# Kernel optimization log

Measured on AMD Instinct MI355X. Metric: run time of the kernel, lower is better.

Reference implementation:

```python
import jax, jax.numpy as jnp
import numpy as np

EPS = 1e-6

def _layernorm(x, g, b):
    mu = jnp.mean(x, axis=-1, keepdims=True)
    var = jnp.mean(jnp.square(x - mu), axis=-1, keepdims=True)
    return (x - mu) * jax.lax.rsqrt(var + EPS) * g + b


def setup_inputs() -> dict:
    key = jax.random.key(0)
    ks = jax.random.split(key, 8)
    B, T, C, H, D = 4096, 64, 256, 4, 64
    s = 0.02
    return {
        "x": jax.random.normal(ks[0], (B, T, C), jnp.float32),
        "ln1_g": jnp.ones((C,), jnp.float32),
        "ln1_b": jnp.zeros((C,), jnp.float32),
        "Wq": jax.random.normal(ks[1], (H, C, D), jnp.float32) * s,
        "Wk": jax.random.normal(ks[2], (H, C, D), jnp.float32) * s,
        "Wv": jax.random.normal(ks[3], (H, C, D), jnp.float32) * s,
        "Wproj": jax.random.normal(ks[4], (C, C), jnp.float32) * s,
        "bproj": jnp.zeros((C,), jnp.float32),
        "ln2_g": jnp.ones((C,), jnp.float32),
        "ln2_b": jnp.zeros((C,), jnp.float32),
        "W1": jax.random.normal(ks[5], (C, 4 * C), jnp.float32) * s,
        "b1": jnp.zeros((4 * C,), jnp.float32),
        "W2": jax.random.normal(ks[6], (4 * C, C), jnp.float32) * s,
        "b2": jnp.zeros((C,), jnp.float32),
    }


def reference(x, ln1_g, ln1_b, Wq, Wk, Wv, Wproj, bproj, ln2_g, ln2_b, W1, b1, W2, b2):
    B, T, C = x.shape
    H, _, D = Wq.shape
    # --- self-attention on pre-LN input (dropout = identity at inference) ---
    h = _layernorm(x, ln1_g, ln1_b)
    q = jnp.einsum('btc,hcd->bhtd', h, Wq)
    k = jnp.einsum('btc,hcd->bhtd', h, Wk)
    v = jnp.einsum('btc,hcd->bhtd', h, Wv)
    scale = jax.lax.rsqrt(jnp.asarray(D, x.dtype))
    wei = jnp.einsum('bhtd,bhsd->bhts', q, k) * scale
    causal = jnp.tril(jnp.ones((T, T), bool))  # matches tril[:T,:T]
    wei = jnp.where(causal, wei, -jnp.inf)
    wei = jax.nn.softmax(wei, axis=-1)
    att = jnp.einsum('bhts,bhsd->bhtd', wei, v)
    att = att.transpose(0, 2, 1, 3).reshape(B, T, H * D)  # concat heads
    sa = att @ Wproj + bproj
    x = x + sa
    # --- feed-forward ---
    h2 = _layernorm(x, ln2_g, ln2_b)
    ff = jax.nn.relu(h2 @ W1 + b1) @ W2 + b2
    return x + ff
```

## Files before the change

### kernel.cpp

```cpp
#include <hip/hip_runtime.h>
#include <hip/hip_bf16.h>


typedef float v4f __attribute__((ext_vector_type(4)));
typedef int   v4i __attribute__((ext_vector_type(4)));
typedef float f4v __attribute__((ext_vector_type(4)));
typedef unsigned long long u64;

#define DEV static __device__ __forceinline__

DEV unsigned short f2bf(float f){
  return __builtin_bit_cast(unsigned short, __float2bfloat16(f));
}

DEV v4f mfma16(v4i a, v4i b, v4f c){
  asm("v_mfma_f32_16x16x32_bf16 %0, %1, %2, %0" : "+v"(c) : "v"(a), "v"(b));
  return c;
}
DEV v4f accfence(v4f c){
  asm("s_nop 7\n\ts_nop 3" : "+v"(c));
  return c;
}

DEV int hoff(int r, int c){ return r*512 + ((c*2) ^ ((r & 7) << 4)); }
DEV int koff(int r, int c){ return r*128 + ((c*2) ^ ((r & 7) << 4)); }
DEV int aoff(int r, int c){ return r*256 + ((c*2) ^ ((r & 7) << 4)); }

DEV u64 pack4(v4f v){
  return (u64)f2bf(v[0]) | ((u64)f2bf(v[1]) << 16)
       | ((u64)f2bf(v[2]) << 32) | ((u64)f2bf(v[3]) << 48);
}

DEV float rsum64(float v){
  #pragma unroll
  for (int k = 1; k < 64; k <<= 1) v += __shfl_xor(v, k);
  return v;
}
DEV float rsum16(float v){
  #pragma unroll
  for (int k = 1; k < 16; k <<= 1) v += __shfl_xor(v, k);
  return v;
}
DEV float rmax16(float v){
  #pragma unroll
  for (int k = 1; k < 16; k <<= 1) v = fmaxf(v, __shfl_xor(v, k));
  return v;
}

__global__ void prep_w(const float* __restrict__ Wq, const float* __restrict__ Wk,
                       const float* __restrict__ Wv, const float* __restrict__ Wp,
                       const float* __restrict__ W1, const float* __restrict__ W2,
                       unsigned short* __restrict__ ws){
  int t = blockIdx.x * 256 + threadIdx.x;
  float v;
  if (t < 196608){
    int seg = t >> 16, r = t & 65535;
    int c = r & 255, d = (r >> 8) & 63, h = r >> 14;
    const float* W = (seg == 0) ? Wq : ((seg == 1) ? Wk : Wv);
    v = W[h*16384 + c*64 + d];
  } else if (t < 262144){
    int r = t - 196608; int n = r >> 8, c = r & 255;
    v = Wp[c*256 + n];
  } else if (t < 524288){
    int r = t - 262144; int n = r >> 8, c = r & 255;
    v = W1[c*1024 + n];
  } else {
    int r = t - 524288; int n = r >> 10, k = r & 1023;
    v = W2[k*256 + n];
  }
  ws[t] = f2bf(v);
}

__global__ __launch_bounds__(256, 2) void attnproj_k(
    const float* __restrict__ x,
    const float* __restrict__ ln1g, const float* __restrict__ ln1b,
    const unsigned short* __restrict__ wqT,
    const unsigned short* __restrict__ wkT,
    const unsigned short* __restrict__ wvT,
    const unsigned short* __restrict__ wpT,
    const float* __restrict__ bpj,
    float* __restrict__ outp)
{
  __shared__ char smb[65536] __attribute__((aligned(16)));
  char* sm = smb;
  const int HLS = 0, QLS = 32768, KLS = 40960, VTLS = 49152, PATLS = 57344;

  const int b = blockIdx.x;
  const float* __restrict__ xb = x + (size_t)b * 16384;
  float* __restrict__ ob = outp + (size_t)b * 16384;
  const int tid = threadIdx.x;
  const int w = tid >> 6, l = tid & 63, m = l & 15, g = l >> 4;
  const v4f zf = {0.f, 0.f, 0.f, 0.f};

  {
    f4v lg = *(const f4v*)(ln1g + 4*l);
    f4v lb = *(const f4v*)(ln1b + 4*l);
    #pragma unroll
    for (int rr = 0; rr < 16; ++rr){
      int r = w*16 + rr;
      f4v xv = *(const f4v*)(xb + r*256 + 4*l);
      float s = xv[0]+xv[1]+xv[2]+xv[3];
      float q = xv[0]*xv[0]+xv[1]*xv[1]+xv[2]*xv[2]+xv[3]*xv[3];
      s = rsum64(s); q = rsum64(q);
      float mu = s * (1.f/256.f);
      float rs = rsqrtf(q * (1.f/256.f) - mu*mu + 1e-6f);
      u64 pk = 0;
      #pragma unroll
      for (int j = 0; j < 4; ++j){
        float hv = (xv[j] - mu) * rs * lg[j] + lb[j];
        pk |= (u64)f2bf(hv) << (16*j);
      }
      *(u64*)(sm + HLS + hoff(r, 4*l)) = pk;
    }
  }
  __syncthreads();

  v4f sa[4][4];
  #pragma unroll
  for (int i = 0; i < 4; ++i){
    #pragma unroll
    for (int j = 0; j < 4; ++j) sa[i][j] = zf;
  }

  #pragma unroll 1
  for (int hh = 0; hh < 4; ++hh){
    {
      const unsigned short* bq = wqT + hh*16384 + (w*16 + m)*256;
      const unsigned short* bk = wkT + hh*16384 + (w*16 + m)*256;
      const unsigned short* bv = wvT + hh*16384 + (w*16 + m)*256;
      v4f qa[4] = {zf,zf,zf,zf}, ka[4] = {zf,zf,zf,zf}, va[4] = {zf,zf,zf,zf};
      #pragma unroll
      for (int ks = 0; ks < 8; ++ks){
        int k0 = ks*32 + 8*g;
        v4i bq4 = *(const v4i*)(bq + k0);
        v4i bk4 = *(const v4i*)(bk + k0);
        v4i bv4 = *(const v4i*)(bv + k0);
        #pragma unroll
        for (int rt = 0; rt < 4; ++rt){
          v4i af = *(const v4i*)(sm + HLS + hoff(rt*16 + m, k0));
          qa[rt] = mfma16(af, bq4, qa[rt]);
          ka[rt] = mfma16(af, bk4, ka[rt]);
          va[rt] = mfma16(af, bv4, va[rt]);
        }
      }
      #pragma unroll
      for (int rt = 0; rt < 4; ++rt){
        qa[rt] = accfence(qa[rt]); ka[rt] = accfence(ka[rt]); va[rt] = accfence(va[rt]);
        #pragma unroll
        for (int j = 0; j < 4; ++j){
          *(unsigned short*)(sm + QLS + koff(rt*16 + 4*g + j, w*16 + m)) = f2bf(qa[rt][j]);
          *(unsigned short*)(sm + KLS + koff(rt*16 + 4*g + j, w*16 + m)) = f2bf(ka[rt][j]);
        }
        *(u64*)(sm + VTLS + koff(w*16 + m, rt*16 + 4*g)) = pack4(va[rt]);
      }
    }
    __syncthreads();

    {
      v4f s4[4] = {zf,zf,zf,zf};
      #pragma unroll
      for (int ks = 0; ks < 2; ++ks){
        int k0 = ks*32 + 8*g;
        v4i qf = *(const v4i*)(sm + QLS + koff(w*16 + m, k0));
        #pragma unroll
        for (int nt = 0; nt < 4; ++nt){
          v4i kf = *(const v4i*)(sm + KLS + koff(nt*16 + m, k0));
          s4[nt] = mfma16(qf, kf, s4[nt]);
        }
      }
      #pragma unroll
      for (int nt = 0; nt < 4; ++nt) s4[nt] = accfence(s4[nt]);
      float mx[4] = {-3e38f, -3e38f, -3e38f, -3e38f};
      #pragma unroll
      for (int nt = 0; nt < 4; ++nt){
        #pragma unroll
        for (int j = 0; j < 4; ++j){
          int t = w*16 + 4*g + j, ss = nt*16 + m;
          float z = s4[nt][j] * 0.125f;
          z = (ss <= t) ? z : -1e30f;
          s4[nt][j] = z;
          mx[j] = fmaxf(mx[j], z);
        }
      }
      #pragma unroll
      for (int j = 0; j < 4; ++j) mx[j] = rmax16(mx[j]);
      float sum[4] = {0.f, 0.f, 0.f, 0.f};
      #pragma unroll
      for (int nt = 0; nt < 4; ++nt){
        #pragma unroll
        for (int j = 0; j < 4; ++j){
          float p = __expf(s4[nt][j] - mx[j]);
          s4[nt][j] = p;
          sum[j] += p;
        }
      }
      #pragma unroll
      for (int j = 0; j < 4; ++j) sum[j] = 1.f / rsum16(sum[j]);
      #pragma unroll
      for (int nt = 0; nt < 4; ++nt){
        #pragma unroll
        for (int j = 0; j < 4; ++j)
          *(unsigned short*)(sm + PATLS + w*2048 + koff(4*g + j, nt*16 + m)) =
              f2bf(s4[nt][j] * sum[j]);
      }
      v4f av[4] = {zf,zf,zf,zf};
      #pragma unroll
      for (int ks = 0; ks < 2; ++ks){
        int k0 = ks*32 + 8*g;
        v4i pf = *(const v4i*)(sm + PATLS + w*2048 + koff(m, k0));
        #pragma unroll
        for (int nt = 0; nt < 4; ++nt){
          v4i vf = *(const v4i*)(sm + VTLS + koff(nt*16 + m, k0));
          av[nt] = mfma16(pf, vf, av[nt]);
        }
      }
      #pragma unroll
      for (int nt = 0; nt < 4; ++nt) av[nt] = accfence(av[nt]);
      #pragma unroll
      for (int nt = 0; nt < 4; ++nt){
        #pragma unroll
        for (int j = 0; j < 4; ++j)
          *(unsigned short*)(sm + PATLS + w*2048 + koff(4*g + j, nt*16 + m)) =
              f2bf(av[nt][j]);
      }
    }
    __syncthreads();

    #pragma unroll
    for (int ks = 0; ks < 2; ++ks){
      int k0 = ks*32 + 8*g;
      v4i af2[4];
      #pragma unroll
      for (int rt = 0; rt < 4; ++rt)
        af2[rt] = *(const v4i*)(sm + PATLS + rt*2048 + koff(m, k0));
      #pragma unroll
      for (int nt = 0; nt < 4; ++nt){
        v4i bp = *(const v4i*)(wpT + (w*64 + nt*16 + m)*256 + hh*64 + k0);
        #pragma unroll
        for (int rt = 0; rt < 4; ++rt) sa[rt][nt] = mfma16(af2[rt], bp, sa[rt][nt]);
      }
    }
  }

  {
    #pragma unroll
    for (int i = 0; i < 4; ++i){
      #pragma unroll
      for (int j = 0; j < 4; ++j) sa[i][j] = accfence(sa[i][j]);
    }
    float bp4[4];
    #pragma unroll
    for (int nt = 0; nt < 4; ++nt) bp4[nt] = bpj[w*64 + nt*16 + m];
    #pragma unroll
    for (int rt = 0; rt < 4; ++rt){
      #pragma unroll
      for (int j = 0; j < 4; ++j){
        int row = rt*16 + 4*g + j;
        #pragma unroll
        for (int nt = 0; nt < 4; ++nt){
          int col = w*64 + nt*16 + m;
          ob[row*256 + col] = xb[row*256 + col] + sa[rt][nt][j] + bp4[nt];
        }
      }
    }
  }
}

__global__ __launch_bounds__(256, 2) void mlp_k(
    const float* __restrict__ ln2g, const float* __restrict__ ln2b,
    const unsigned short* __restrict__ w1T,
    const float* __restrict__ b1,
    const unsigned short* __restrict__ w2T,
    const float* __restrict__ b2,
    float* __restrict__ outp)
{
  __shared__ char smb[65536] __attribute__((aligned(16)));
  char* sm = smb;
  const int HLS = 0;
  const int ACT0 = 32768, ACT1 = 49152;
  const int b = blockIdx.x;
  float* __restrict__ ob = outp + (size_t)b * 16384;
  const int tid = threadIdx.x;
  const int w = tid >> 6, l = tid & 63, m = l & 15, g = l >> 4;
  const v4f zf = {0.f, 0.f, 0.f, 0.f};

  {
    f4v lg = *(const f4v*)(ln2g + 4*l);
    f4v lb = *(const f4v*)(ln2b + 4*l);
    #pragma unroll
    for (int rr = 0; rr < 16; ++rr){
      int r = w*16 + rr;
      f4v xv = *(const f4v*)(ob + r*256 + 4*l);
      float s = xv[0]+xv[1]+xv[2]+xv[3];
      float q = xv[0]*xv[0]+xv[1]*xv[1]+xv[2]*xv[2]+xv[3]*xv[3];
      s = rsum64(s); q = rsum64(q);
      float mu = s * (1.f/256.f);
      float rs = rsqrtf(q * (1.f/256.f) - mu*mu + 1e-6f);
      u64 pk = 0;
      #pragma unroll
      for (int j = 0; j < 4; ++j){
        float hv = (xv[j] - mu) * rs * lg[j] + lb[j];
        pk |= (u64)f2bf(hv) << (16*j);
      }
      *(u64*)(sm + HLS + hoff(r, 4*l)) = pk;
    }
  }
  __syncthreads();

  v4f ff[4][4];
  #pragma unroll
  for (int i = 0; i < 4; ++i){
    #pragma unroll
    for (int j = 0; j < 4; ++j) ff[i][j] = zf;
  }

  #pragma unroll 1
  for (int ch = 0; ch < 8; ++ch){
    const int ACT = (ch & 1) ? ACT1 : ACT0;
    v4f a1[4][2];
    #pragma unroll
    for (int i = 0; i < 4; ++i){ a1[i][0] = zf; a1[i][1] = zf; }
    const unsigned short* w1a = w1T + (ch*128 + w*32 +      m)*256;
    const unsigned short* w1b = w1T + (ch*128 + w*32 + 16 + m)*256;
    #pragma unroll
    for (int ks = 0; ks < 8; ++ks){
      int k0 = ks*32 + 8*g;
      v4i bw0 = *(const v4i*)(w1a + k0);
      v4i bw1 = *(const v4i*)(w1b + k0);
      #pragma unroll
      for (int rt = 0; rt < 4; ++rt){
        v4i af = *(const v4i*)(sm + HLS + hoff(rt*16 + m, k0));
        a1[rt][0] = mfma16(af, bw0, a1[rt][0]);
        a1[rt][1] = mfma16(af, bw1, a1[rt][1]);
      }
    }
    float b1v[2] = { b1[ch*128 + w*32 + m], b1[ch*128 + w*32 + 16 + m] };
    #pragma unroll
    for (int i = 0; i < 4; ++i){ a1[i][0] = accfence(a1[i][0]); a1[i][1] = accfence(a1[i][1]); }
    #pragma unroll
    for (int rt = 0; rt < 4; ++rt){
      #pragma unroll
      for (int j = 0; j < 4; ++j){
        int row = rt*16 + 4*g + j;
        #pragma unroll
        for (int nt = 0; nt < 2; ++nt){
          float v = fmaxf(a1[rt][nt][j] + b1v[nt], 0.f);
          *(unsigned short*)(sm + ACT + aoff(row, w*32 + nt*16 + m)) = f2bf(v);
        }
      }
    }
    __syncthreads();
    #pragma unroll
    for (int ks = 0; ks < 4; ++ks){
      int k0 = ks*32 + 8*g;
      v4i af[4];
      #pragma unroll
      for (int rt = 0; rt < 4; ++rt)
        af[rt] = *(const v4i*)(sm + ACT + aoff(rt*16 + m, k0));
      #pragma unroll
      for (int nt = 0; nt < 4; ++nt){
        v4i bw = *(const v4i*)(w2T + (w*64 + nt*16 + m)*1024 + ch*128 + k0);
        #pragma unroll
        for (int rt = 0; rt < 4; ++rt) ff[rt][nt] = mfma16(af[rt], bw, ff[rt][nt]);
      }
    }
  }

  {
    float b2v[4];
    #pragma unroll
    for (int nt = 0; nt < 4; ++nt) b2v[nt] = b2[w*64 + nt*16 + m];
    #pragma unroll
    for (int i = 0; i < 4; ++i){
      #pragma unroll
      for (int j = 0; j < 4; ++j) ff[i][j] = accfence(ff[i][j]);
    }
    #pragma unroll
    for (int rt = 0; rt < 4; ++rt){
      #pragma unroll
      for (int j = 0; j < 4; ++j){
        int row = rt*16 + 4*g + j;
        #pragma unroll
        for (int nt = 0; nt < 4; ++nt){
          int col = w*64 + nt*16 + m;
          ob[row*256 + col] += ff[rt][nt][j] + b2v[nt];
        }
      }
    }
  }
}

extern "C" void kernel_launch(void* const* d_in, const int* in_sizes, int n_in,
                              void* d_out, int out_size, void* d_ws, size_t ws_size,
                              hipStream_t stream) {
  const float* x    = (const float*)d_in[0];
  const float* ln1g = (const float*)d_in[1];
  const float* ln1b = (const float*)d_in[2];
  const float* Wq   = (const float*)d_in[3];
  const float* Wk   = (const float*)d_in[4];
  const float* Wv   = (const float*)d_in[5];
  const float* Wp   = (const float*)d_in[6];
  const float* bpj  = (const float*)d_in[7];
  const float* ln2g = (const float*)d_in[8];
  const float* ln2b = (const float*)d_in[9];
  const float* W1   = (const float*)d_in[10];
  const float* b1   = (const float*)d_in[11];
  const float* W2   = (const float*)d_in[12];
  const float* b2   = (const float*)d_in[13];
  unsigned short* ws = (unsigned short*)d_ws;
  float* outp = (float*)d_out;

  prep_w<<<3072, 256, 0, stream>>>(Wq, Wk, Wv, Wp, W1, W2, ws);
  attnproj_k<<<4096, 256, 0, stream>>>(x, ln1g, ln1b,
                                       ws, ws + 65536, ws + 131072, ws + 196608,
                                       bpj, outp);
  mlp_k<<<4096, 256, 0, stream>>>(ln2g, ln2b, ws + 262144, b1,
                                  ws + 524288, b2, outp);
}
```

Baseline: 965.8 us.

## Retile MLP kernel to 128 rows per 512-thread block, add lightweight barriers

Result: faster. 897.8 us (-7.0%).

```diff
diff --git a/kernel.cpp b/kernel.cpp
--- a/kernel.cpp
+++ b/kernel.cpp
@@ -13,6 +13,10 @@
   return __builtin_bit_cast(unsigned short, __float2bfloat16(f));
 }
 
+DEV void bar(){
+  asm volatile("s_waitcnt lgkmcnt(0)\n\ts_barrier" ::: "memory");
+}
+
 DEV v4f mfma16(v4i a, v4i b, v4f c){
   asm("v_mfma_f32_16x16x32_bf16 %0, %1, %2, %0" : "+v"(c) : "v"(a), "v"(b));
   return c;
@@ -24,7 +28,6 @@
 
 DEV int hoff(int r, int c){ return r*512 + ((c*2) ^ ((r & 7) << 4)); }
 DEV int koff(int r, int c){ return r*128 + ((c*2) ^ ((r & 7) << 4)); }
-DEV int aoff(int r, int c){ return r*256 + ((c*2) ^ ((r & 7) << 4)); }
 
 DEV u64 pack4(v4f v){
   return (u64)f2bf(v[0]) | ((u64)f2bf(v[1]) << 16)
@@ -113,7 +116,7 @@
       *(u64*)(sm + HLS + hoff(r, 4*l)) = pk;
     }
   }
-  __syncthreads();
+  bar();
 
   v4f sa[4][4];
   #pragma unroll
@@ -154,7 +157,7 @@
         *(u64*)(sm + VTLS + koff(w*16 + m, rt*16 + 4*g)) = pack4(va[rt]);
       }
     }
-    __syncthreads();
+    bar();
 
     {
       v4f s4[4] = {zf,zf,zf,zf};
@@ -224,7 +227,7 @@
               f2bf(av[nt][j]);
       }
     }
-    __syncthreads();
+    bar();
 
     #pragma unroll
     for (int ks = 0; ks < 2; ++ks){
@@ -266,7 +269,8 @@
   }
 }
 
-__global__ __launch_bounds__(256, 2) void mlp_k(
+#define MLP_LDS 131072
+__global__ __launch_bounds__(512, 1) void mlp_k(
     const float* __restrict__ ln2g, const float* __restrict__ ln2b,
     const unsigned short* __restrict__ w1T,
     const float* __restrict__ b1,
@@ -274,12 +278,10 @@
     const float* __restrict__ b2,
     float* __restrict__ outp)
 {
-  __shared__ char smb[65536] __attribute__((aligned(16)));
-  char* sm = smb;
-  const int HLS = 0;
-  const int ACT0 = 32768, ACT1 = 49152;
-  const int b = blockIdx.x;
-  float* __restrict__ ob = outp + (size_t)b * 16384;
+  extern __shared__ char sm[];
+  const int HLS = 0, ACT = 65536;
+  const int bb = blockIdx.x;
+  float* __restrict__ ob = outp + (size_t)bb * 32768;
   const int tid = threadIdx.x;
   const int w = tid >> 6, l = tid & 63, m = l & 15, g = l >> 4;
   const v4f zf = {0.f, 0.f, 0.f, 0.f};
@@ -305,84 +307,77 @@
       *(u64*)(sm + HLS + hoff(r, 4*l)) = pk;
     }
   }
-  __syncthreads();
-
-  v4f ff[4][4];
+  bar();
+
+  v4f ff[8][2];
   #pragma unroll
-  for (int i = 0; i < 4; ++i){
-    #pragma unroll
-    for (int j = 0; j < 4; ++j) ff[i][j] = zf;
-  }
+  for (int i = 0; i < 8; ++i){ ff[i][0] = zf; ff[i][1] = zf; }
 
   #pragma unroll 1
-  for (int ch = 0; ch < 8; ++ch){
-    const int ACT = (ch & 1) ? ACT1 : ACT0;
-    v4f a1[4][2];
-    #pragma unroll
-    for (int i = 0; i < 4; ++i){ a1[i][0] = zf; a1[i][1] = zf; }
-    const unsigned short* w1a = w1T + (ch*128 + w*32 +      m)*256;
-    const unsigned short* w1b = w1T + (ch*128 + w*32 + 16 + m)*256;
+  for (int ch = 0; ch < 4; ++ch){
+    v4f a1[8][2];
+    #pragma unroll
+    for (int i = 0; i < 8; ++i){ a1[i][0] = zf; a1[i][1] = zf; }
+    const unsigned short* w1a = w1T + (ch*256 + w*32 +      m)*256;
+    const unsigned short* w1b = w1T + (ch*256 + w*32 + 16 + m)*256;
     #pragma unroll
     for (int ks = 0; ks < 8; ++ks){
       int k0 = ks*32 + 8*g;
       v4i bw0 = *(const v4i*)(w1a + k0);
       v4i bw1 = *(const v4i*)(w1b + k0);
       #pragma unroll
-      for (int rt = 0; rt < 4; ++rt){
+      for (int rt = 0; rt < 8; ++rt){
         v4i af = *(const v4i*)(sm + HLS + hoff(rt*16 + m, k0));
         a1[rt][0] = mfma16(af, bw0, a1[rt][0]);
         a1[rt][1] = mfma16(af, bw1, a1[rt][1]);
       }
     }
-    float b1v[2] = { b1[ch*128 + w*32 + m], b1[ch*128 + w*32 + 16 + m] };
-    #pragma unroll
-    for (int i = 0; i < 4; ++i){ a1[i][0] = accfence(a1[i][0]); a1[i][1] = accfence(a1[i][1]); }
-    #pragma unroll
-    for (int rt = 0; rt < 4; ++rt){
+    float b1v[2] = { b1[ch*256 + w*32 + m], b1[ch*256 + w*32 + 16 + m] };
+    #pragma unroll
+    for (int i = 0; i < 8; ++i){ a1[i][0] = accfence(a1[i][0]); a1[i][1] = accfence(a1[i][1]); }
+    #pragma unroll
+    for (int rt = 0; rt < 8; ++rt){
       #pragma unroll
       for (int j = 0; j < 4; ++j){
         int row = rt*16 + 4*g + j;
         #pragma unroll
         for (int nt = 0; nt < 2; ++nt){
           float v = fmaxf(a1[rt][nt][j] + b1v[nt], 0.f);
-          *(unsigned short*)(sm + ACT + aoff(row, w*32 + nt*16 + m)) = f2bf(v);
-        }
-      }
-    }
-    __syncthreads();
-    #pragma unroll
-    for (int ks = 0; ks < 4; ++ks){
+          *(unsigned short*)(sm + ACT + hoff(row, w*32 + nt*16 + m)) = f2bf(v);
+        }
+      }
+    }
+    bar();
+
+    #pragma unroll
+    for (int ks = 0; ks < 8; ++ks){
       int k0 = ks*32 + 8*g;
-      v4i af[4];
-      #pragma unroll
-      for (int rt = 0; rt < 4; ++rt)
-        af[rt] = *(const v4i*)(sm + ACT + aoff(rt*16 + m, k0));
-      #pragma unroll
-      for (int nt = 0; nt < 4; ++nt){
-        v4i bw = *(const v4i*)(w2T + (w*64 + nt*16 + m)*1024 + ch*128 + k0);
-        #pragma unroll
-        for (int rt = 0; rt < 4; ++rt) ff[rt][nt] = mfma16(af[rt], bw, ff[rt][nt]);
-      }
-    }
+      v4i af[8];
+      #pragma unroll
+      for (int rt = 0; rt < 8; ++rt)
+        af[rt] = *(const v4i*)(sm + ACT + hoff(rt*16 + m, k0));
+      #pragma unroll
+      for (int nt = 0; nt < 2; ++nt){
+        v4i bw = *(const v4i*)(w2T + (w*32 + nt*16 + m)*1024 + ch*256 + k0);
+        #pragma unroll
+        for (int rt = 0; rt < 8; ++rt) ff[rt][nt] = mfma16(af[rt], bw, ff[rt][nt]);
+      }
+    }
+    bar();
   }
 
   {
-    float b2v[4];
-    #pragma unroll
-    for (int nt = 0; nt < 4; ++nt) b2v[nt] = b2[w*64 + nt*16 + m];
-    #pragma unroll
-    for (int i = 0; i < 4; ++i){
-      #pragma unroll
-      for (int j = 0; j < 4; ++j) ff[i][j] = accfence(ff[i][j]);
-    }
-    #pragma unroll
-    for (int rt = 0; rt < 4; ++rt){
+    float b2v[2] = { b2[w*32 + m], b2[w*32 + 16 + m] };
+    #pragma unroll
+    for (int i = 0; i < 8; ++i){ ff[i][0] = accfence(ff[i][0]); ff[i][1] = accfence(ff[i][1]); }
+    #pragma unroll
+    for (int rt = 0; rt < 8; ++rt){
       #pragma unroll
       for (int j = 0; j < 4; ++j){
         int row = rt*16 + 4*g + j;
         #pragma unroll
-        for (int nt = 0; nt < 4; ++nt){
-          int col = w*64 + nt*16 + m;
+        for (int nt = 0; nt < 2; ++nt){
+          int col = w*32 + nt*16 + m;
           ob[row*256 + col] += ff[rt][nt][j] + b2v[nt];
         }
       }
@@ -410,10 +405,13 @@
   unsigned short* ws = (unsigned short*)d_ws;
   float* outp = (float*)d_out;
 
+  hipFuncSetAttribute((const void*)mlp_k,
+                      hipFuncAttributeMaxDynamicSharedMemorySize, MLP_LDS);
+
   prep_w<<<3072, 256, 0, stream>>>(Wq, Wk, Wv, Wp, W1, W2, ws);
   attnproj_k<<<4096, 256, 0, stream>>>(x, ln1g, ln1b,
                                        ws, ws + 65536, ws + 131072, ws + 196608,
                                        bpj, outp);
-  mlp_k<<<4096, 256, 0, stream>>>(ln2g, ln2b, ws + 262144, b1,
-                                  ws + 524288, b2, outp);
-}
+  mlp_k<<<2048, 512, MLP_LDS, stream>>>(ln2g, ln2b, ws + 262144, b1,
+                                        ws + 524288, b2, outp);
+}
```

## Shrink MLP hidden chunk to 64 with single LDS buffer and lighter barriers

Applied to the files above, without the earlier changes.

Result: slower. 1.038 ms (+7.5%).

```diff
diff --git a/kernel.cpp b/kernel.cpp
--- a/kernel.cpp
+++ b/kernel.cpp
@@ -13,6 +13,10 @@
   return __builtin_bit_cast(unsigned short, __float2bfloat16(f));
 }
 
+DEV void bar(){
+  asm volatile("s_waitcnt lgkmcnt(0)\n\ts_barrier" ::: "memory");
+}
+
 DEV v4f mfma16(v4i a, v4i b, v4f c){
   asm("v_mfma_f32_16x16x32_bf16 %0, %1, %2, %0" : "+v"(c) : "v"(a), "v"(b));
   return c;
@@ -24,7 +28,6 @@
 
 DEV int hoff(int r, int c){ return r*512 + ((c*2) ^ ((r & 7) << 4)); }
 DEV int koff(int r, int c){ return r*128 + ((c*2) ^ ((r & 7) << 4)); }
-DEV int aoff(int r, int c){ return r*256 + ((c*2) ^ ((r & 7) << 4)); }
 
 DEV u64 pack4(v4f v){
   return (u64)f2bf(v[0]) | ((u64)f2bf(v[1]) << 16)
@@ -113,7 +116,7 @@
       *(u64*)(sm + HLS + hoff(r, 4*l)) = pk;
     }
   }
-  __syncthreads();
+  bar();
 
   v4f sa[4][4];
   #pragma unroll
@@ -154,7 +157,7 @@
         *(u64*)(sm + VTLS + koff(w*16 + m, rt*16 + 4*g)) = pack4(va[rt]);
       }
     }
-    __syncthreads();
+    bar();
 
     {
       v4f s4[4] = {zf,zf,zf,zf};
@@ -224,7 +227,7 @@
               f2bf(av[nt][j]);
       }
     }
-    __syncthreads();
+    bar();
 
     #pragma unroll
     for (int ks = 0; ks < 2; ++ks){
@@ -274,10 +277,9 @@
     const float* __restrict__ b2,
     float* __restrict__ outp)
 {
-  __shared__ char smb[65536] __attribute__((aligned(16)));
+  __shared__ char smb[40960] __attribute__((aligned(16)));
   char* sm = smb;
-  const int HLS = 0;
-  const int ACT0 = 32768, ACT1 = 49152;
+  const int HLS = 0, ACT = 32768;
   const int b = blockIdx.x;
   float* __restrict__ ob = outp + (size_t)b * 16384;
   const int tid = threadIdx.x;
@@ -305,7 +307,7 @@
       *(u64*)(sm + HLS + hoff(r, 4*l)) = pk;
     }
   }
-  __syncthreads();
+  bar();
 
   v4f ff[4][4];
   #pragma unroll
@@ -315,55 +317,47 @@
   }
 
   #pragma unroll 1
-  for (int ch = 0; ch < 8; ++ch){
-    const int ACT = (ch & 1) ? ACT1 : ACT0;
-    v4f a1[4][2];
-    #pragma unroll
-    for (int i = 0; i < 4; ++i){ a1[i][0] = zf; a1[i][1] = zf; }
-    const unsigned short* w1a = w1T + (ch*128 + w*32 +      m)*256;
-    const unsigned short* w1b = w1T + (ch*128 + w*32 + 16 + m)*256;
+  for (int ch = 0; ch < 16; ++ch){
+    v4f a1[4] = {zf, zf, zf, zf};
+    const unsigned short* w1p = w1T + (ch*64 + w*16 + m)*256;
     #pragma unroll
     for (int ks = 0; ks < 8; ++ks){
       int k0 = ks*32 + 8*g;
-      v4i bw0 = *(const v4i*)(w1a + k0);
-      v4i bw1 = *(const v4i*)(w1b + k0);
+      v4i bw = *(const v4i*)(w1p + k0);
       #pragma unroll
       for (int rt = 0; rt < 4; ++rt){
         v4i af = *(const v4i*)(sm + HLS + hoff(rt*16 + m, k0));
-        a1[rt][0] = mfma16(af, bw0, a1[rt][0]);
-        a1[rt][1] = mfma16(af, bw1, a1[rt][1]);
-      }
-    }
-    float b1v[2] = { b1[ch*128 + w*32 + m], b1[ch*128 + w*32 + 16 + m] };
-    #pragma unroll
-    for (int i = 0; i < 4; ++i){ a1[i][0] = accfence(a1[i][0]); a1[i][1] = accfence(a1[i][1]); }
+        a1[rt] = mfma16(af, bw, a1[rt]);
+      }
+    }
+    float b1v = b1[ch*64 + w*16 + m];
     #pragma unroll
     for (int rt = 0; rt < 4; ++rt){
+      a1[rt] = accfence(a1[rt]);
       #pragma unroll
       for (int j = 0; j < 4; ++j){
         int row = rt*16 + 4*g + j;
-        #pragma unroll
-        for (int nt = 0; nt < 2; ++nt){
-          float v = fmaxf(a1[rt][nt][j] + b1v[nt], 0.f);
-          *(unsigned short*)(sm + ACT + aoff(row, w*32 + nt*16 + m)) = f2bf(v);
-        }
-      }
-    }
-    __syncthreads();
-    #pragma unroll
-    for (int ks = 0; ks < 4; ++ks){
+        float v = fmaxf(a1[rt][j] + b1v, 0.f);
+        *(unsigned short*)(sm + ACT + koff(row, w*16 + m)) = f2bf(v);
+      }
+    }
+    bar();
+
+    #pragma unroll
+    for (int ks = 0; ks < 2; ++ks){
       int k0 = ks*32 + 8*g;
       v4i af[4];
       #pragma unroll
       for (int rt = 0; rt < 4; ++rt)
-        af[rt] = *(const v4i*)(sm + ACT + aoff(rt*16 + m, k0));
-      #pragma unroll
-      for (int nt = 0; nt < 4; ++nt){
-        v4i bw = *(const v4i*)(w2T + (w*64 + nt*16 + m)*1024 + ch*128 + k0);
+        af[rt] = *(const v4i*)(sm + ACT + koff(rt*16 + m, k0));
+      #pragma unroll
+      for (int nt = 0; nt < 4; ++nt){
+        v4i bw = *(const v4i*)(w2T + (w*64 + nt*16 + m)*1024 + ch*64 + k0);
         #pragma unroll
         for (int rt = 0; rt < 4; ++rt) ff[rt][nt] = mfma16(af[rt], bw, ff[rt][nt]);
       }
     }
+    bar();
   }
 
   {
```
